# Performance work log

Measured on AMD Instinct MI355X. Metric: run time of the kernel, lower is better.

## Reference

```python
import jax, jax.numpy as jnp
import numpy as np

N, K = 200000, 16
C_IN = 4           # in_channels (head stage)
H1, H2 = 16, 32    # nbr_hidden_channels//2, nbr_hidden_channels
C_OUT = 64         # channel_list[0]
HEAD = 256         # head_channels
EPS = 1e-5


def _bn(x, g, b):
    # train-mode BatchNorm1d over the row (point/neighbor) axis
    m = jnp.mean(x, axis=0)
    v = jnp.var(x, axis=0)
    return (x - m) * jax.lax.rsqrt(v + EPS) * g + b


def setup_inputs() -> dict:
    key = jax.random.key(0)
    ks = jax.random.split(key, 8)

    def lin(k, fan_in, fan_out):
        bound = 1.0 / np.sqrt(fan_in)  # torch Linear default init
        return jax.random.uniform(k, (fan_in, fan_out), minval=-bound, maxval=bound, dtype=jnp.float32)

    return {
        "p": jax.random.normal(ks[0], (N, 3), dtype=jnp.float32),
        "f": jax.random.normal(ks[1], (N, C_IN), dtype=jnp.float32),
        "group_idx": jax.random.randint(ks[2], (N, K), 0, N),
        "w1": lin(ks[3], 3 + C_IN, H1),
        "g1": jnp.ones((H1,), jnp.float32),
        "b1": jnp.zeros((H1,), jnp.float32),
        "w2": lin(ks[4], H1, H2),
        "g2": jnp.ones((H2,), jnp.float32),
        "b2": jnp.zeros((H2,), jnp.float32),
        "w3": lin(ks[5], H2, C_OUT),
        "g_nbr": 0.8 * jnp.ones((C_OUT,), jnp.float32),  # nn.init.constant_(nbr_bn.weight, 0.8)
        "b_nbr": jnp.zeros((C_OUT,), jnp.float32),
        "g_post": jnp.ones((C_OUT,), jnp.float32),       # (channel_list[0]/out_channels)**0.5 == 1.0
        "b_post": jnp.zeros((C_OUT,), jnp.float32),
        "w_post": lin(ks[6], C_OUT, HEAD),
    }


def reference(p, f, group_idx, w1, g1, b1, w2, g2, b2, w3, g_nbr, b_nbr, g_post, b_post, w_post):
    # neighbor gather: relative coords and features  -> (N, K, 3), (N, K, C_IN)
    p_nbr = p[group_idx] - p[:, None, :]
    f_nbr = f[group_idx]
    x = jnp.concatenate([p_nbr, f_nbr], axis=-1).reshape(N * K, 3 + C_IN)
    # nbr_embed: Linear-BN-GELU x2 + Linear (all no-bias linears)
    x = jax.nn.gelu(_bn(x @ w1, g1, b1), approximate=False)
    x = jax.nn.gelu(_bn(x @ w2, g2, b2), approximate=False)
    x = (x @ w3).reshape(N, K, C_OUT).max(axis=1)  # max-pool over K neighbors
    # nbr_proj is Identity for the head stage; nbr_bn then f = f_nbr
    x = _bn(x, g_nbr, b_nbr)
    # post_proj: BN + Linear(C_OUT -> HEAD, no bias)
    out = _bn(x, g_post, b_post) @ w_post
    return out
```

## Files before the change

kernel.cpp:

```cpp
#include <hip/hip_runtime.h>
#include <cmath>

#define NPTS  200000
#define KNBR  16
#define MROWS 3200000
#define EPSB  1e-5f
#define H2LD  260

__device__ __forceinline__ float gelu_f(float x) {
    return 0.5f * x * (1.0f + erff(x * 0.70710678118654752f));
}

__global__ __launch_bounds__(256) void k_stats1(
    const float* __restrict__ p, const float4* __restrict__ f,
    const int* __restrict__ gidx, float* __restrict__ stats)
{
    __shared__ float red[4 * 35];

    float acc[35];
#pragma unroll
    for (int c = 0; c < 35; c++) acc[c] = 0.f;

    int stride = gridDim.x * 256;
    for (int r = blockIdx.x * 256 + threadIdx.x; r < MROWS; r += stride) {
        int n = r >> 4;
        int idx = gidx[r];
        float4 fv = f[idx];
        float x[7];
        x[0] = p[idx * 3 + 0] - p[n * 3 + 0];
        x[1] = p[idx * 3 + 1] - p[n * 3 + 1];
        x[2] = p[idx * 3 + 2] - p[n * 3 + 2];
        x[3] = fv.x; x[4] = fv.y; x[5] = fv.z; x[6] = fv.w;
#pragma unroll
        for (int i = 0; i < 7; i++) acc[i] += x[i];
        int t = 7;
#pragma unroll
        for (int i = 0; i < 7; i++)
#pragma unroll
            for (int l = i; l < 7; l++) { acc[t] = fmaf(x[i], x[l], acc[t]); t++; }
    }
    int lane = threadIdx.x & 63, wv = threadIdx.x >> 6;
#pragma unroll
    for (int c = 0; c < 35; c++) {
        float v = acc[c];
        v += __shfl_down(v, 32); v += __shfl_down(v, 16); v += __shfl_down(v, 8);
        v += __shfl_down(v, 4);  v += __shfl_down(v, 2);  v += __shfl_down(v, 1);
        if (lane == 0) red[wv * 35 + c] = v;
    }
    __syncthreads();
    for (int c = threadIdx.x; c < 35; c += 256)
        atomicAdd(&stats[c], red[c] + red[35 + c] + red[70 + c] + red[105 + c]);
}

__global__ void k_fin1(const float* __restrict__ stats, const float* __restrict__ w1,
                       const float* __restrict__ g, const float* __restrict__ b,
                       float* __restrict__ scsh)
{
    int j = threadIdx.x;
    if (j < 16) {
        const float invM = 1.0f / (float)MROWS;
        float w[7];
#pragma unroll
        for (int i = 0; i < 7; i++) w[i] = w1[i * 16 + j];
        float m = 0.f;
#pragma unroll
        for (int i = 0; i < 7; i++) m = fmaf(w[i], stats[i], m);
        m *= invM;
        float e2 = 0.f;
        int t = 7;
#pragma unroll
        for (int i = 0; i < 7; i++)
#pragma unroll
            for (int l = i; l < 7; l++) {
                float coeff = (i == l) ? 1.0f : 2.0f;
                e2 = fmaf(coeff * w[i] * w[l], stats[t], e2);
                t++;
            }
        e2 *= invM;
        float v = e2 - m * m;
        float sc = g[j] * rsqrtf(v + EPSB);
        scsh[j] = sc;
        scsh[16 + j] = fmaf(-m, sc, b[j]);
    }
}

__global__ __launch_bounds__(256) void k_stats2a(
    const float* __restrict__ p, const float4* __restrict__ f,
    const int* __restrict__ gidx, const float* __restrict__ w1,
    const float* __restrict__ scsh1, float* __restrict__ stats)
{
    __shared__ __align__(16) float w1s[112];
    __shared__ float sc1s[16], sh1s[16];
    __shared__ float red[4 * 100];
    for (int i = threadIdx.x; i < 112; i += 256) w1s[i] = w1[i];
    if (threadIdx.x < 16) {
        sc1s[threadIdx.x] = scsh1[threadIdx.x];
        sh1s[threadIdx.x] = scsh1[16 + threadIdx.x];
    }
    __syncthreads();
    const float4* w1v = (const float4*)w1s;

    float acc[100];
#pragma unroll
    for (int c = 0; c < 100; c++) acc[c] = 0.f;

    int stride = gridDim.x * 256;
    for (int r = blockIdx.x * 256 + threadIdx.x; r < MROWS; r += stride) {
        int n = r >> 4;
        int idx = gidx[r];
        float4 fv = f[idx];
        float x[7];
        x[0] = p[idx * 3 + 0] - p[n * 3 + 0];
        x[1] = p[idx * 3 + 1] - p[n * 3 + 1];
        x[2] = p[idx * 3 + 2] - p[n * 3 + 2];
        x[3] = fv.x; x[4] = fv.y; x[5] = fv.z; x[6] = fv.w;
        float h1[16];
#pragma unroll
        for (int j0 = 0; j0 < 16; j0 += 4) {
            float y0 = 0.f, y1 = 0.f, y2 = 0.f, y3 = 0.f;
#pragma unroll
            for (int i = 0; i < 7; i++) {
                float4 w = w1v[i * 4 + (j0 >> 2)];
                float xi = x[i];
                y0 = fmaf(xi, w.x, y0); y1 = fmaf(xi, w.y, y1);
                y2 = fmaf(xi, w.z, y2); y3 = fmaf(xi, w.w, y3);
            }
            h1[j0 + 0] = gelu_f(fmaf(y0, sc1s[j0 + 0], sh1s[j0 + 0]));
            h1[j0 + 1] = gelu_f(fmaf(y1, sc1s[j0 + 1], sh1s[j0 + 1]));
            h1[j0 + 2] = gelu_f(fmaf(y2, sc1s[j0 + 2], sh1s[j0 + 2]));
            h1[j0 + 3] = gelu_f(fmaf(y3, sc1s[j0 + 3], sh1s[j0 + 3]));
        }
        int t = 0;
#pragma unroll
        for (int i = 0; i < 8; i++)
#pragma unroll
            for (int l = i; l < 16; l++) { acc[t] = fmaf(h1[i], h1[l], acc[t]); t++; }
    }
    int lane = threadIdx.x & 63, wv = threadIdx.x >> 6;
#pragma unroll
    for (int c = 0; c < 100; c++) {
        float v = acc[c];
        v += __shfl_down(v, 32); v += __shfl_down(v, 16); v += __shfl_down(v, 8);
        v += __shfl_down(v, 4);  v += __shfl_down(v, 2);  v += __shfl_down(v, 1);
        if (lane == 0) red[wv * 100 + c] = v;
    }
    __syncthreads();
    for (int c = threadIdx.x; c < 100; c += 256)
        atomicAdd(&stats[c], red[c] + red[100 + c] + red[200 + c] + red[300 + c]);
}

__global__ __launch_bounds__(256) void k_stats2b(
    const float* __restrict__ p, const float4* __restrict__ f,
    const int* __restrict__ gidx, const float* __restrict__ w1,
    const float* __restrict__ scsh1, float* __restrict__ stats)
{
    __shared__ __align__(16) float w1s[112];
    __shared__ float sc1s[16], sh1s[16];
    __shared__ float red[4 * 52];
    for (int i = threadIdx.x; i < 112; i += 256) w1s[i] = w1[i];
    if (threadIdx.x < 16) {
        sc1s[threadIdx.x] = scsh1[threadIdx.x];
        sh1s[threadIdx.x] = scsh1[16 + threadIdx.x];
    }
    __syncthreads();
    const float4* w1v = (const float4*)w1s;

    float acc[52];
#pragma unroll
    for (int c = 0; c < 52; c++) acc[c] = 0.f;

    int stride = gridDim.x * 256;
    for (int r = blockIdx.x * 256 + threadIdx.x; r < MROWS; r += stride) {
        int n = r >> 4;
        int idx = gidx[r];
        float4 fv = f[idx];
        float x[7];
        x[0] = p[idx * 3 + 0] - p[n * 3 + 0];
        x[1] = p[idx * 3 + 1] - p[n * 3 + 1];
        x[2] = p[idx * 3 + 2] - p[n * 3 + 2];
        x[3] = fv.x; x[4] = fv.y; x[5] = fv.z; x[6] = fv.w;
        float h1[16];
#pragma unroll
        for (int j0 = 0; j0 < 16; j0 += 4) {
            float y0 = 0.f, y1 = 0.f, y2 = 0.f, y3 = 0.f;
#pragma unroll
            for (int i = 0; i < 7; i++) {
                float4 w = w1v[i * 4 + (j0 >> 2)];
                float xi = x[i];
                y0 = fmaf(xi, w.x, y0); y1 = fmaf(xi, w.y, y1);
                y2 = fmaf(xi, w.z, y2); y3 = fmaf(xi, w.w, y3);
            }
            h1[j0 + 0] = gelu_f(fmaf(y0, sc1s[j0 + 0], sh1s[j0 + 0]));
            h1[j0 + 1] = gelu_f(fmaf(y1, sc1s[j0 + 1], sh1s[j0 + 1]));
            h1[j0 + 2] = gelu_f(fmaf(y2, sc1s[j0 + 2], sh1s[j0 + 2]));
            h1[j0 + 3] = gelu_f(fmaf(y3, sc1s[j0 + 3], sh1s[j0 + 3]));
        }
#pragma unroll
        for (int i = 0; i < 16; i++) acc[i] += h1[i];
        int t = 16;
#pragma unroll
        for (int i = 8; i < 16; i++)
#pragma unroll
            for (int l = i; l < 16; l++) { acc[t] = fmaf(h1[i], h1[l], acc[t]); t++; }
    }
    int lane = threadIdx.x & 63, wv = threadIdx.x >> 6;
#pragma unroll
    for (int c = 0; c < 52; c++) {
        float v = acc[c];
        v += __shfl_down(v, 32); v += __shfl_down(v, 16); v += __shfl_down(v, 8);
        v += __shfl_down(v, 4);  v += __shfl_down(v, 2);  v += __shfl_down(v, 1);
        if (lane == 0) red[wv * 52 + c] = v;
    }
    __syncthreads();
    for (int c = threadIdx.x; c < 52; c += 256)
        atomicAdd(&stats[100 + c], red[c] + red[52 + c] + red[104 + c] + red[156 + c]);
}

__global__ void k_fin2(const float* __restrict__ stats, const float* __restrict__ w2,
                       const float* __restrict__ g, const float* __restrict__ b,
                       float* __restrict__ scsh)
{
    int j = threadIdx.x;
    if (j < 32) {
        const float invM = 1.0f / (float)MROWS;
        float w[16];
#pragma unroll
        for (int i = 0; i < 16; i++) w[i] = w2[i * 32 + j];
        float m = 0.f;
#pragma unroll
        for (int i = 0; i < 16; i++) m = fmaf(w[i], stats[100 + i], m);
        m *= invM;
        float e2 = 0.f;
        int t = 0;
#pragma unroll
        for (int i = 0; i < 8; i++)
#pragma unroll
            for (int l = i; l < 16; l++) {
                float coeff = (i == l) ? 1.0f : 2.0f;
                e2 = fmaf(coeff * w[i] * w[l], stats[t], e2);
                t++;
            }
        t = 116;
#pragma unroll
        for (int i = 8; i < 16; i++)
#pragma unroll
            for (int l = i; l < 16; l++) {
                float coeff = (i == l) ? 1.0f : 2.0f;
                e2 = fmaf(coeff * w[i] * w[l], stats[t], e2);
                t++;
            }
        e2 *= invM;
        float v = e2 - m * m;
        float sc = g[j] * rsqrtf(v + EPSB);
        scsh[j] = sc;
        scsh[32 + j] = fmaf(-m, sc, b[j]);
    }
}

__global__ __launch_bounds__(256) void k_pool2(
    const float* __restrict__ p, const float4* __restrict__ f,
    const int* __restrict__ gidx,
    const float* __restrict__ w1, const float* __restrict__ w2,
    const float* __restrict__ w3,
    const float* __restrict__ scsh1, const float* __restrict__ scsh2,
    float* __restrict__ stats, float* __restrict__ pooled)
{
    __shared__ __align__(16) float w1s[112];
    __shared__ __align__(16) float w2s[512];
    __shared__ __align__(16) float w3s[2048];
    __shared__ __align__(16) float h2t[32 * H2LD];
    __shared__ float sc1s[16], sh1s[16], sc2s[32], sh2s[32];
    __shared__ float reds[256];
    __shared__ float redq[256];
    int tid = threadIdx.x;
    for (int i = tid; i < 112; i += 256) w1s[i] = w1[i];
    for (int i = tid; i < 512; i += 256) w2s[i] = w2[i];
    for (int i = tid; i < 2048; i += 256) w3s[i] = w3[i];
    if (tid < 16) { sc1s[tid] = scsh1[tid]; sh1s[tid] = scsh1[16 + tid]; }
    if (tid < 32) { sc2s[tid] = scsh2[tid]; sh2s[tid] = scsh2[32 + tid]; }
    __syncthreads();

    const float4* w1v = (const float4*)w1s;
    const float4* w2v = (const float4*)w2s;
    const float4* w3v = (const float4*)w3s;

    int lane = tid & 63;
    int pt = tid >> 4;
    int cc = tid & 15;

    float s0 = 0.f, s1 = 0.f, s2 = 0.f, s3 = 0.f;
    float q0 = 0.f, q1 = 0.f, q2 = 0.f, q3 = 0.f;

#pragma unroll 1
    for (int it = 0; it < 4; it++) {
        int r = it * 800000 + blockIdx.x * 256 + tid;
        int n = r >> 4;
        int idx = gidx[r];
        float4 fv = f[idx];
        float x[7];
        x[0] = p[idx * 3 + 0] - p[n * 3 + 0];
        x[1] = p[idx * 3 + 1] - p[n * 3 + 1];
        x[2] = p[idx * 3 + 2] - p[n * 3 + 2];
        x[3] = fv.x; x[4] = fv.y; x[5] = fv.z; x[6] = fv.w;

        float h1[16];
#pragma unroll
        for (int j0 = 0; j0 < 16; j0 += 4) {
            float y0 = 0.f, y1 = 0.f, y2 = 0.f, y3 = 0.f;
#pragma unroll
            for (int i = 0; i < 7; i++) {
                float4 w = w1v[i * 4 + (j0 >> 2)];
                float xi = x[i];
                y0 = fmaf(xi, w.x, y0); y1 = fmaf(xi, w.y, y1);
                y2 = fmaf(xi, w.z, y2); y3 = fmaf(xi, w.w, y3);
            }
            h1[j0 + 0] = gelu_f(fmaf(y0, sc1s[j0 + 0], sh1s[j0 + 0]));
            h1[j0 + 1] = gelu_f(fmaf(y1, sc1s[j0 + 1], sh1s[j0 + 1]));
            h1[j0 + 2] = gelu_f(fmaf(y2, sc1s[j0 + 2], sh1s[j0 + 2]));
            h1[j0 + 3] = gelu_f(fmaf(y3, sc1s[j0 + 3], sh1s[j0 + 3]));
        }
#pragma unroll
        for (int j0 = 0; j0 < 32; j0 += 4) {
            float y0 = 0.f, y1 = 0.f, y2 = 0.f, y3 = 0.f;
#pragma unroll
            for (int i = 0; i < 16; i++) {
                float4 w = w2v[i * 8 + (j0 >> 2)];
                float hi = h1[i];
                y0 = fmaf(hi, w.x, y0); y1 = fmaf(hi, w.y, y1);
                y2 = fmaf(hi, w.z, y2); y3 = fmaf(hi, w.w, y3);
            }
            h2t[(j0 + 0) * H2LD + tid] = gelu_f(fmaf(y0, sc2s[j0 + 0], sh2s[j0 + 0]));
            h2t[(j0 + 1) * H2LD + tid] = gelu_f(fmaf(y1, sc2s[j0 + 1], sh2s[j0 + 1]));
            h2t[(j0 + 2) * H2LD + tid] = gelu_f(fmaf(y2, sc2s[j0 + 2], sh2s[j0 + 2]));
            h2t[(j0 + 3) * H2LD + tid] = gelu_f(fmaf(y3, sc2s[j0 + 3], sh2s[j0 + 3]));
        }
        __syncthreads();

        float m0 = -3.0e38f, m1 = -3.0e38f, m2 = -3.0e38f, m3 = -3.0e38f;
#pragma unroll 1
        for (int qd = 0; qd < 4; qd++) {
            int rb = (pt << 4) + (qd << 2);
            float a00 = 0.f, a01 = 0.f, a02 = 0.f, a03 = 0.f;
            float a10 = 0.f, a11 = 0.f, a12 = 0.f, a13 = 0.f;
            float a20 = 0.f, a21 = 0.f, a22 = 0.f, a23 = 0.f;
            float a30 = 0.f, a31 = 0.f, a32 = 0.f, a33 = 0.f;
#pragma unroll 8
            for (int i = 0; i < 32; i++) {
                float4 hv = *(const float4*)&h2t[i * H2LD + rb];
                float4 wf = w3v[i * 16 + cc];
                a00 = fmaf(hv.x, wf.x, a00); a01 = fmaf(hv.x, wf.y, a01);
                a02 = fmaf(hv.x, wf.z, a02); a03 = fmaf(hv.x, wf.w, a03);
                a10 = fmaf(hv.y, wf.x, a10); a11 = fmaf(hv.y, wf.y, a11);
                a12 = fmaf(hv.y, wf.z, a12); a13 = fmaf(hv.y, wf.w, a13);
                a20 = fmaf(hv.z, wf.x, a20); a21 = fmaf(hv.z, wf.y, a21);
                a22 = fmaf(hv.z, wf.z, a22); a23 = fmaf(hv.z, wf.w, a23);
                a30 = fmaf(hv.w, wf.x, a30); a31 = fmaf(hv.w, wf.y, a31);
                a32 = fmaf(hv.w, wf.z, a32); a33 = fmaf(hv.w, wf.w, a33);
            }
            m0 = fmaxf(fmaxf(fmaxf(m0, a00), fmaxf(a10, a20)), a30);
            m1 = fmaxf(fmaxf(fmaxf(m1, a01), fmaxf(a11, a21)), a31);
            m2 = fmaxf(fmaxf(fmaxf(m2, a02), fmaxf(a12, a22)), a32);
            m3 = fmaxf(fmaxf(fmaxf(m3, a03), fmaxf(a13, a23)), a33);
        }
        int np = it * 50000 + blockIdx.x * 16 + pt;
        *(float4*)&pooled[(size_t)np * 64 + cc * 4] = make_float4(m0, m1, m2, m3);
        s0 += m0; q0 = fmaf(m0, m0, q0);
        s1 += m1; q1 = fmaf(m1, m1, q1);
        s2 += m2; q2 = fmaf(m2, m2, q2);
        s3 += m3; q3 = fmaf(m3, m3, q3);
        __syncthreads();
    }

    s0 += __shfl_down(s0, 32); s0 += __shfl_down(s0, 16);
    s1 += __shfl_down(s1, 32); s1 += __shfl_down(s1, 16);
    s2 += __shfl_down(s2, 32); s2 += __shfl_down(s2, 16);
    s3 += __shfl_down(s3, 32); s3 += __shfl_down(s3, 16);
    q0 += __shfl_down(q0, 32); q0 += __shfl_down(q0, 16);
    q1 += __shfl_down(q1, 32); q1 += __shfl_down(q1, 16);
    q2 += __shfl_down(q2, 32); q2 += __shfl_down(q2, 16);
    q3 += __shfl_down(q3, 32); q3 += __shfl_down(q3, 16);
    int wv = tid >> 6;
    if (lane < 16) {
        reds[wv * 64 + lane * 4 + 0] = s0;
        reds[wv * 64 + lane * 4 + 1] = s1;
        reds[wv * 64 + lane * 4 + 2] = s2;
        reds[wv * 64 + lane * 4 + 3] = s3;
        redq[wv * 64 + lane * 4 + 0] = q0;
        redq[wv * 64 + lane * 4 + 1] = q1;
        redq[wv * 64 + lane * 4 + 2] = q2;
        redq[wv * 64 + lane * 4 + 3] = q3;
    }
    __syncthreads();
    if (tid < 64) {
        atomicAdd(&stats[tid],
                  reds[tid] + reds[64 + tid] + reds[128 + tid] + reds[192 + tid]);
        atomicAdd(&stats[64 + tid],
                  redq[tid] + redq[64 + tid] + redq[128 + tid] + redq[192 + tid]);
    }
}

__global__ void k_fin3(const float* __restrict__ stats,
                       const float* __restrict__ g_nbr, const float* __restrict__ g_post,
                       const float* __restrict__ b_post, float* __restrict__ scsh)
{
    int j = threadIdx.x;
    if (j < 64) {
        float m = stats[j] * (1.0f / NPTS);
        float v = stats[64 + j] * (1.0f / NPTS) - m * m;
        float a1 = g_nbr[j] * rsqrtf(v + EPSB);
        float s3 = g_post[j] * a1 * rsqrtf(fmaf(a1 * a1, v, EPSB));
        scsh[j] = s3;
        scsh[64 + j] = fmaf(-m, s3, b_post[j]);
    }
}

__global__ __launch_bounds__(256) void k_head(
    const float* __restrict__ pooled, const float* __restrict__ scsh3,
    const float* __restrict__ wpost, float* __restrict__ out)
{
    __shared__ float rowbuf[512];
    __shared__ float s3s[64], c3s[64];
    int tid = threadIdx.x;
    if (tid < 64) { s3s[tid] = scsh3[tid]; c3s[tid] = scsh3[64 + tid]; }
    float wcol[64];
#pragma unroll
    for (int j = 0; j < 64; j++) wcol[j] = wpost[j * 256 + tid];
    __syncthreads();

    const int nchunks = NPTS / 8;
    for (int c = blockIdx.x; c < nchunks; c += gridDim.x) {
        int n0 = c * 8;
#pragma unroll
        for (int t = tid; t < 512; t += 256) {
            int rr = t >> 6, j = t & 63;
            rowbuf[t] = fmaf(pooled[(size_t)(n0 + rr) * 64 + j], s3s[j], c3s[j]);
        }
        __syncthreads();
#pragma unroll
        for (int rr = 0; rr < 8; rr++) {
            float acc = 0.f;
#pragma unroll
            for (int j = 0; j < 64; j++) acc = fmaf(rowbuf[rr * 64 + j], wcol[j], acc);
            out[(size_t)(n0 + rr) * 256 + tid] = acc;
        }
        __syncthreads();
    }
}

extern "C" void kernel_launch(void* const* d_in, const int* in_sizes, int n_in,
                              void* d_out, int out_size, void* d_ws, size_t ws_size,
                              hipStream_t stream)
{
    const float*  p    = (const float*)d_in[0];
    const float4* f    = (const float4*)d_in[1];
    const int*    gidx = (const int*)d_in[2];
    const float*  w1   = (const float*)d_in[3];
    const float*  g1   = (const float*)d_in[4];
    const float*  b1   = (const float*)d_in[5];
    const float*  w2   = (const float*)d_in[6];
    const float*  g2   = (const float*)d_in[7];
    const float*  b2   = (const float*)d_in[8];
    const float*  w3   = (const float*)d_in[9];
    const float*  gn   = (const float*)d_in[10];
    const float*  gp   = (const float*)d_in[12];
    const float*  bp   = (const float*)d_in[13];
    const float*  wp   = (const float*)d_in[14];
    float* out = (float*)d_out;
    float* ws  = (float*)d_ws;

    float* stats1 = ws;
    float* scsh1  = ws + 40;
    float* stats2 = ws + 80;
    float* scsh2  = ws + 240;
    float* stats3 = ws + 304;
    float* scsh3  = ws + 432;
    float* pooled = ws + 1024;

    hipMemsetAsync(d_ws, 0, 2048, stream);
    k_stats1<<<2048, 256, 0, stream>>>(p, f, gidx, stats1);
    k_fin1<<<1, 64, 0, stream>>>(stats1, w1, g1, b1, scsh1);
    k_stats2a<<<2048, 256, 0, stream>>>(p, f, gidx, w1, scsh1, stats2);
    k_stats2b<<<2048, 256, 0, stream>>>(p, f, gidx, w1, scsh1, stats2);
    k_fin2<<<1, 64, 0, stream>>>(stats2, w2, g2, b2, scsh2);
    k_pool2<<<3125, 256, 0, stream>>>(p, f, gidx, w1, w2, w3, scsh1, scsh2, stats3, pooled);
    k_fin3<<<1, 64, 0, stream>>>(stats3, gn, gp, bp, scsh3);
    k_head<<<1024, 256, 0, stream>>>(pooled, scsh3, wp, out);
}
```

Before: 1.259 ms.

## Pack point coords and features into interleaved float4 buffer; rebalance stats2 split

Adds a pack kernel that interleaves each point's xyz and 4 features into two float4s, so the three stats kernels gather one 32-byte record per neighbor instead of scalar p loads plus a separate f load. It also moves the split of second-order h1 products between k_stats2a and k_stats2b (81 and 71 accumulators instead of 100 and 52) to even out register pressure, and updates k_fin2 indexing to match. The packed buffer sits in workspace at the same offset as the pooled buffer, which is only written later by k_pool2, so the reuse looks safe. k_pool2 still reads the original p and f arrays.

Measured after the change: 1.287 ms. 1.02x slower.

```diff
diff --git a/kernel.cpp b/kernel.cpp
--- a/kernel.cpp
+++ b/kernel.cpp
@@ -11,9 +11,22 @@
     return 0.5f * x * (1.0f + erff(x * 0.70710678118654752f));
 }
 
+__global__ __launch_bounds__(256) void k_pack(
+    const float* __restrict__ p, const float4* __restrict__ f,
+    float4* __restrict__ pk)
+{
+    int n = blockIdx.x * 256 + threadIdx.x;
+    if (n < NPTS) {
+        float4 a;
+        a.x = p[n * 3 + 0]; a.y = p[n * 3 + 1]; a.z = p[n * 3 + 2]; a.w = 0.f;
+        pk[2 * n]     = a;
+        pk[2 * n + 1] = f[n];
+    }
+}
+
 __global__ __launch_bounds__(256) void k_stats1(
-    const float* __restrict__ p, const float4* __restrict__ f,
-    const int* __restrict__ gidx, float* __restrict__ stats)
+    const float4* __restrict__ pk, const int* __restrict__ gidx,
+    float* __restrict__ stats)
 {
     __shared__ float red[4 * 35];
 
@@ -25,12 +38,12 @@
     for (int r = blockIdx.x * 256 + threadIdx.x; r < MROWS; r += stride) {
         int n = r >> 4;
         int idx = gidx[r];
-        float4 fv = f[idx];
+        float4 pa = pk[2 * idx];
+        float4 fb = pk[2 * idx + 1];
+        float4 pc = pk[2 * n];
         float x[7];
-        x[0] = p[idx * 3 + 0] - p[n * 3 + 0];
-        x[1] = p[idx * 3 + 1] - p[n * 3 + 1];
-        x[2] = p[idx * 3 + 2] - p[n * 3 + 2];
-        x[3] = fv.x; x[4] = fv.y; x[5] = fv.z; x[6] = fv.w;
+        x[0] = pa.x - pc.x; x[1] = pa.y - pc.y; x[2] = pa.z - pc.z;
+        x[3] = fb.x; x[4] = fb.y; x[5] = fb.z; x[6] = fb.w;
 #pragma unroll
         for (int i = 0; i < 7; i++) acc[i] += x[i];
         int t = 7;
@@ -85,13 +98,13 @@
 }
 
 __global__ __launch_bounds__(256) void k_stats2a(
-    const float* __restrict__ p, const float4* __restrict__ f,
-    const int* __restrict__ gidx, const float* __restrict__ w1,
-    const float* __restrict__ scsh1, float* __restrict__ stats)
+    const float4* __restrict__ pk, const int* __restrict__ gidx,
+    const float* __restrict__ w1, const float* __restrict__ scsh1,
+    float* __restrict__ stats)
 {
     __shared__ __align__(16) float w1s[112];
     __shared__ float sc1s[16], sh1s[16];
-    __shared__ float red[4 * 100];
+    __shared__ float red[4 * 81];
     for (int i = threadIdx.x; i < 112; i += 256) w1s[i] = w1[i];
     if (threadIdx.x < 16) {
         sc1s[threadIdx.x] = scsh1[threadIdx.x];
@@ -100,20 +113,20 @@
     __syncthreads();
     const float4* w1v = (const float4*)w1s;
 
-    float acc[100];
-#pragma unroll
-    for (int c = 0; c < 100; c++) acc[c] = 0.f;
+    float acc[81];
+#pragma unroll
+    for (int c = 0; c < 81; c++) acc[c] = 0.f;
 
     int stride = gridDim.x * 256;
     for (int r = blockIdx.x * 256 + threadIdx.x; r < MROWS; r += stride) {
         int n = r >> 4;
         int idx = gidx[r];
-        float4 fv = f[idx];
+        float4 pa = pk[2 * idx];
+        float4 fb = pk[2 * idx + 1];
+        float4 pc = pk[2 * n];
         float x[7];
-        x[0] = p[idx * 3 + 0] - p[n * 3 + 0];
-        x[1] = p[idx * 3 + 1] - p[n * 3 + 1];
-        x[2] = p[idx * 3 + 2] - p[n * 3 + 2];
-        x[3] = fv.x; x[4] = fv.y; x[5] = fv.z; x[6] = fv.w;
+        x[0] = pa.x - pc.x; x[1] = pa.y - pc.y; x[2] = pa.z - pc.z;
+        x[3] = fb.x; x[4] = fb.y; x[5] = fb.z; x[6] = fb.w;
         float h1[16];
 #pragma unroll
         for (int j0 = 0; j0 < 16; j0 += 4) {
@@ -132,31 +145,31 @@
         }
         int t = 0;
 #pragma unroll
-        for (int i = 0; i < 8; i++)
+        for (int i = 0; i < 6; i++)
 #pragma unroll
             for (int l = i; l < 16; l++) { acc[t] = fmaf(h1[i], h1[l], acc[t]); t++; }
     }
     int lane = threadIdx.x & 63, wv = threadIdx.x >> 6;
 #pragma unroll
-    for (int c = 0; c < 100; c++) {
+    for (int c = 0; c < 81; c++) {
         float v = acc[c];
         v += __shfl_down(v, 32); v += __shfl_down(v, 16); v += __shfl_down(v, 8);
         v += __shfl_down(v, 4);  v += __shfl_down(v, 2);  v += __shfl_down(v, 1);
-        if (lane == 0) red[wv * 100 + c] = v;
-    }
-    __syncthreads();
-    for (int c = threadIdx.x; c < 100; c += 256)
-        atomicAdd(&stats[c], red[c] + red[100 + c] + red[200 + c] + red[300 + c]);
+        if (lane == 0) red[wv * 81 + c] = v;
+    }
+    __syncthreads();
+    for (int c = threadIdx.x; c < 81; c += 256)
+        atomicAdd(&stats[c], red[c] + red[81 + c] + red[162 + c] + red[243 + c]);
 }
 
 __global__ __launch_bounds__(256) void k_stats2b(
-    const float* __restrict__ p, const float4* __restrict__ f,
-    const int* __restrict__ gidx, const float* __restrict__ w1,
-    const float* __restrict__ scsh1, float* __restrict__ stats)
+    const float4* __restrict__ pk, const int* __restrict__ gidx,
+    const float* __restrict__ w1, const float* __restrict__ scsh1,
+    float* __restrict__ stats)
 {
     __shared__ __align__(16) float w1s[112];
     __shared__ float sc1s[16], sh1s[16];
-    __shared__ float red[4 * 52];
+    __shared__ float red[4 * 71];
     for (int i = threadIdx.x; i < 112; i += 256) w1s[i] = w1[i];
     if (threadIdx.x < 16) {
         sc1s[threadIdx.x] = scsh1[threadIdx.x];
@@ -165,20 +178,20 @@
     __syncthreads();
     const float4* w1v = (const float4*)w1s;
 
-    float acc[52];
-#pragma unroll
-    for (int c = 0; c < 52; c++) acc[c] = 0.f;
+    float acc[71];
+#pragma unroll
+    for (int c = 0; c < 71; c++) acc[c] = 0.f;
 
     int stride = gridDim.x * 256;
     for (int r = blockIdx.x * 256 + threadIdx.x; r < MROWS; r += stride) {
         int n = r >> 4;
         int idx = gidx[r];
-        float4 fv = f[idx];
+        float4 pa = pk[2 * idx];
+        float4 fb = pk[2 * idx + 1];
+        float4 pc = pk[2 * n];
         float x[7];
-        x[0] = p[idx * 3 + 0] - p[n * 3 + 0];
-        x[1] = p[idx * 3 + 1] - p[n * 3 + 1];
-        x[2] = p[idx * 3 + 2] - p[n * 3 + 2];
-        x[3] = fv.x; x[4] = fv.y; x[5] = fv.z; x[6] = fv.w;
+        x[0] = pa.x - pc.x; x[1] = pa.y - pc.y; x[2] = pa.z - pc.z;
+        x[3] = fb.x; x[4] = fb.y; x[5] = fb.z; x[6] = fb.w;
         float h1[16];
 #pragma unroll
         for (int j0 = 0; j0 < 16; j0 += 4) {
@@ -199,21 +212,21 @@
         for (int i = 0; i < 16; i++) acc[i] += h1[i];
         int t = 16;
 #pragma unroll
-        for (int i = 8; i < 16; i++)
+        for (int i = 6; i < 16; i++)
 #pragma unroll
             for (int l = i; l < 16; l++) { acc[t] = fmaf(h1[i], h1[l], acc[t]); t++; }
     }
     int lane = threadIdx.x & 63, wv = threadIdx.x >> 6;
 #pragma unroll
-    for (int c = 0; c < 52; c++) {
+    for (int c = 0; c < 71; c++) {
         float v = acc[c];
         v += __shfl_down(v, 32); v += __shfl_down(v, 16); v += __shfl_down(v, 8);
         v += __shfl_down(v, 4);  v += __shfl_down(v, 2);  v += __shfl_down(v, 1);
-        if (lane == 0) red[wv * 52 + c] = v;
-    }
-    __syncthreads();
-    for (int c = threadIdx.x; c < 52; c += 256)
-        atomicAdd(&stats[100 + c], red[c] + red[52 + c] + red[104 + c] + red[156 + c]);
+        if (lane == 0) red[wv * 71 + c] = v;
+    }
+    __syncthreads();
+    for (int c = threadIdx.x; c < 71; c += 256)
+        atomicAdd(&stats[81 + c], red[c] + red[71 + c] + red[142 + c] + red[213 + c]);
 }
 
 __global__ void k_fin2(const float* __restrict__ stats, const float* __restrict__ w2,
@@ -228,21 +241,21 @@
         for (int i = 0; i < 16; i++) w[i] = w2[i * 32 + j];
         float m = 0.f;
 #pragma unroll
-        for (int i = 0; i < 16; i++) m = fmaf(w[i], stats[100 + i], m);
+        for (int i = 0; i < 16; i++) m = fmaf(w[i], stats[81 + i], m);
         m *= invM;
         float e2 = 0.f;
         int t = 0;
 #pragma unroll
-        for (int i = 0; i < 8; i++)
+        for (int i = 0; i < 6; i++)
 #pragma unroll
             for (int l = i; l < 16; l++) {
                 float coeff = (i == l) ? 1.0f : 2.0f;
                 e2 = fmaf(coeff * w[i] * w[l], stats[t], e2);
                 t++;
             }
-        t = 116;
-#pragma unroll
-        for (int i = 8; i < 16; i++)
+        t = 97;
+#pragma unroll
+        for (int i = 6; i < 16; i++)
 #pragma unroll
             for (int l = i; l < 16; l++) {
                 float coeff = (i == l) ? 1.0f : 2.0f;
@@ -475,12 +488,14 @@
     float* stats3 = ws + 304;
     float* scsh3  = ws + 432;
     float* pooled = ws + 1024;
+    float4* pk    = (float4*)(ws + 1024);
 
     hipMemsetAsync(d_ws, 0, 2048, stream);
-    k_stats1<<<2048, 256, 0, stream>>>(p, f, gidx, stats1);
+    k_pack<<<(NPTS + 255) / 256, 256, 0, stream>>>(p, f, pk);
+    k_stats1<<<2048, 256, 0, stream>>>(pk, gidx, stats1);
     k_fin1<<<1, 64, 0, stream>>>(stats1, w1, g1, b1, scsh1);
-    k_stats2a<<<2048, 256, 0, stream>>>(p, f, gidx, w1, scsh1, stats2);
-    k_stats2b<<<2048, 256, 0, stream>>>(p, f, gidx, w1, scsh1, stats2);
+    k_stats2a<<<2048, 256, 0, stream>>>(pk, gidx, w1, scsh1, stats2);
+    k_stats2b<<<2048, 256, 0, stream>>>(pk, gidx, w1, scsh1, stats2);
     k_fin2<<<1, 64, 0, stream>>>(stats2, w2, g2, b2, scsh2);
     k_pool2<<<3125, 256, 0, stream>>>(p, f, gidx, w1, w2, w3, scsh1, scsh2, stats3, pooled);
     k_fin3<<<1, 64, 0, stream>>>(stats3, gn, gp, bp, scsh3);
```
